# Kernel tuning notes

Hardware: AMD Instinct MI355X
Metric: run time of the kernel (lower is better)

The kernel has to match this reference:

```python
import jax, jax.numpy as jnp
import numpy as np

B, L, C, H, Wd = 256, 64, 256, 32, 32  # batch, num_filts, code_dim, height, width

def setup_inputs() -> dict:
    key = jax.random.key(0)
    k1, k2 = jax.random.split(key)
    code = jax.random.normal(k1, (B, L, C), dtype=jnp.float32)
    # stacked per-filter weights: weights[l].weight has shape [code_dim, H*W]
    W = jax.random.normal(k2, (L, C, H * Wd), dtype=jnp.float32) * (1.0 / np.sqrt(C))
    return {"code": code, "W": W}

def reference(code, W):
    # Original: for each filter l, x_hat[:, l] = code[:, l, :] @ weights[l].weight
    # (F.linear(x, weight.t()) == x @ weight). Fuse into one batched GEMM.
    # code: [B, L, C], W: [L, C, HW] -> out: [B, L, HW]
    x_hat = jnp.einsum('blc,lcd->bld', code, W)
    return x_hat.reshape(code.shape[0], W.shape[0], H, Wd)
```

## Files before the change

### kernel.cpp

```cpp
#include <hip/hip_runtime.h>
#include <hip/hip_bf16.h>

#define B_  256
#define L_  64
#define C_  256
#define HW_ 1024

typedef float  floatx4 __attribute__((ext_vector_type(4)));
typedef __bf16 bf16x8  __attribute__((ext_vector_type(8)));
typedef __bf16 bf16x4  __attribute__((ext_vector_type(4)));

#define LDT_A 72
#define LDB_ROW 128

#define BARRIER_LDS() asm volatile("s_waitcnt lgkmcnt(0)\n\ts_barrier" ::: "memory")

__device__ __forceinline__ int bswz(int n) { return (n ^ (n >> 2)) & 7; }

__global__ __launch_bounds__(512, 4)
void gld_mfma_kernel(const float* __restrict__ code,
                     const float* __restrict__ W,
                     float* __restrict__ out)
{
    const int tid = threadIdx.x;

    const int id  = blockIdx.x;
    const int ll  = id & 7;
    const int inr = id >> 3;
    const int m0  = (inr & 1) * 128;
    const int n0  = ((inr >> 1) & 7) * 128;
    const int l   = (inr >> 4) * 8 + ll;

    __shared__ __bf16 Alds[128 * LDT_A];
    __shared__ unsigned char Blds[128 * LDB_ROW];

    const int lane = tid & 63;
    const int wave = tid >> 6;
    const int wm = (wave >> 2) * 64;
    const int wn = (wave & 3) * 32;

    floatx4 acc[4][2];
    #pragma unroll
    for (int i = 0; i < 4; ++i)
        #pragma unroll
        for (int j = 0; j < 2; ++j)
            acc[i][j] = (floatx4)0.0f;

    const int a_row = tid >> 4;
    const int a_kc  = (tid & 15) * 4;
    const int b_i  = tid & 31;
    const int b_c8 = tid >> 5;

    const float* aBase = code + (size_t)m0 * (L_ * C_) + (size_t)l * C_ + a_kc;
    const float* wBase = W + (size_t)l * (C_ * HW_) + (size_t)(4 * b_c8) * HW_ + n0 + 4 * b_i;

    floatx4 Areg[4];
    floatx4 Breg[2][4];

    #pragma unroll
    for (int p = 0; p < 4; ++p)
        Areg[p] = *(const floatx4*)(aBase + (size_t)(p * 32 + a_row) * (L_ * C_));
    #pragma unroll
    for (int r = 0; r < 4; ++r)
        Breg[0][r] = *(const floatx4*)(wBase + (size_t)r * HW_);
    #pragma unroll
    for (int r = 0; r < 4; ++r)
        Breg[1][r] = *(const floatx4*)(wBase + (size_t)(64 + r) * HW_);

    int bwaddr[4];
    #pragma unroll
    for (int j = 0; j < 4; ++j) {
        const int row = 4 * b_i + j;
        bwaddr[j] = row * LDB_ROW + (((b_c8 >> 1) ^ bswz(row)) << 4) + ((b_c8 & 1) << 3);
    }

    #pragma unroll
    for (int kb = 0; kb < C_; kb += 64) {
        const int pb = (kb >> 6) & 1;

        #pragma unroll
        for (int j = 0; j < 4; ++j) {
            bf16x4 h;
            h.x = (__bf16)Breg[pb][0][j]; h.y = (__bf16)Breg[pb][1][j];
            h.z = (__bf16)Breg[pb][2][j]; h.w = (__bf16)Breg[pb][3][j];
            *(bf16x4*)&Blds[bwaddr[j]] = h;
        }
        #pragma unroll
        for (int p = 0; p < 4; ++p) {
            bf16x4 h;
            h.x = (__bf16)Areg[p].x; h.y = (__bf16)Areg[p].y;
            h.z = (__bf16)Areg[p].z; h.w = (__bf16)Areg[p].w;
            *(bf16x4*)&Alds[(p * 32 + a_row) * LDT_A + a_kc] = h;
        }

        if (kb + 64 < C_) {
            #pragma unroll
            for (int p = 0; p < 4; ++p)
                Areg[p] = *(const floatx4*)(aBase + (size_t)(p * 32 + a_row) * (L_ * C_) + (kb + 64));
        }
        if (kb + 128 < C_) {
            #pragma unroll
            for (int r = 0; r < 4; ++r)
                Breg[pb][r] = *(const floatx4*)(wBase + (size_t)(kb + 128 + r) * HW_);
        }

        BARRIER_LDS();

        #pragma unroll
        for (int ks = 0; ks < 2; ++ks) {
            bf16x8 af[4], bfr[2];
            const int koff = ks * 32 + (lane >> 4) * 8;
            #pragma unroll
            for (int i = 0; i < 4; ++i)
                af[i] = *(const bf16x8*)&Alds[(wm + i * 16 + (lane & 15)) * LDT_A + koff];
            #pragma unroll
            for (int j = 0; j < 2; ++j) {
                const int n = wn + j * 16 + (lane & 15);
                bfr[j] = *(const bf16x8*)&Blds[n * LDB_ROW + (((koff >> 3) ^ bswz(n)) << 4)];
            }
            #pragma unroll
            for (int i = 0; i < 4; ++i)
                #pragma unroll
                for (int j = 0; j < 2; ++j)
                    acc[i][j] = __builtin_amdgcn_mfma_f32_16x16x32_bf16(af[i], bfr[j], acc[i][j], 0, 0, 0);
        }

        BARRIER_LDS();
    }

    const int col0 = lane & 15;
    const int row0 = (lane >> 4) * 4;
    #pragma unroll
    for (int i = 0; i < 4; ++i) {
        #pragma unroll
        for (int j = 0; j < 2; ++j) {
            const int m = m0 + wm + i * 16 + row0;
            const int n = n0 + wn + j * 16 + col0;
            float* o = out + (size_t)m * (L_ * HW_) + (size_t)l * HW_ + n;
            #pragma unroll
            for (int r = 0; r < 4; ++r)
                o[(size_t)r * (L_ * HW_)] = acc[i][j][r];
        }
    }
}

extern "C" void kernel_launch(void* const* d_in, const int* in_sizes, int n_in,
                              void* d_out, int out_size, void* d_ws, size_t ws_size,
                              hipStream_t stream) {
    const float* code = (const float*)d_in[0];
    const float* W    = (const float*)d_in[1];
    float* out        = (float*)d_out;

    gld_mfma_kernel<<<dim3(1024), 512, 0, stream>>>(code, W, out);
}
```

Measured before the change: 133.7 us.

## Enlarge block tile to 256x256 covering full batch per filter

Each block now computes all 256 batch rows and 256 output columns for one filter, with each wave holding a 128x64 accumulator tile. This removes redundant global reads of code and W across blocks and raises MFMA work per LDS load. A is moved to the swizzled LDS layout used for B. In exchange the grid shrinks to 256 blocks with larger register and LDS use, which lowers occupancy, and W prefetch depth drops to a single stage.

Result: slower. 139.5 us (+4.4%).

```diff
diff --git a/kernel.cpp b/kernel.cpp
--- a/kernel.cpp
+++ b/kernel.cpp
@@ -10,40 +10,39 @@
 typedef __bf16 bf16x8  __attribute__((ext_vector_type(8)));
 typedef __bf16 bf16x4  __attribute__((ext_vector_type(4)));
 
-#define LDT_A 72
-#define LDB_ROW 128
-
 #define BARRIER_LDS() asm volatile("s_waitcnt lgkmcnt(0)\n\ts_barrier" ::: "memory")
 
 __device__ __forceinline__ int bswz(int n) { return (n ^ (n >> 2)) & 7; }
+__device__ __forceinline__ int lds_addr(int row, int c16, int off) {
+    return row * 128 + ((c16 ^ bswz(row)) << 4) + off;
+}
 
-__global__ __launch_bounds__(512, 4)
+__global__ __launch_bounds__(512, 2)
 void gld_mfma_kernel(const float* __restrict__ code,
                      const float* __restrict__ W,
                      float* __restrict__ out)
 {
     const int tid = threadIdx.x;
 
-    const int id  = blockIdx.x;
-    const int ll  = id & 7;
-    const int inr = id >> 3;
-    const int m0  = (inr & 1) * 128;
-    const int n0  = ((inr >> 1) & 7) * 128;
-    const int l   = (inr >> 4) * 8 + ll;
+    const int id   = blockIdx.x;
+    const int ll   = id & 7;
+    const int rest = id >> 3;
+    const int n0   = (rest & 3) * 256;
+    const int l    = (rest >> 2) * 8 + ll;
 
-    __shared__ __bf16 Alds[128 * LDT_A];
-    __shared__ unsigned char Blds[128 * LDB_ROW];
+    __shared__ unsigned char Alds[256 * 128];
+    __shared__ unsigned char Blds[256 * 128];
 
     const int lane = tid & 63;
     const int wave = tid >> 6;
-    const int wm = (wave >> 2) * 64;
-    const int wn = (wave & 3) * 32;
+    const int wm = (wave >> 2) * 128;
+    const int wn = (wave & 3) * 64;
 
-    floatx4 acc[4][2];
+    floatx4 acc[8][4];
     #pragma unroll
-    for (int i = 0; i < 4; ++i)
+    for (int i = 0; i < 8; ++i)
         #pragma unroll
-        for (int j = 0; j < 2; ++j)
+        for (int j = 0; j < 4; ++j)
             acc[i][j] = (floatx4)0.0f;
 
     const int a_row = tid >> 4;
@@ -51,77 +50,70 @@
     const int b_i  = tid & 31;
     const int b_c8 = tid >> 5;
 
-    const float* aBase = code + (size_t)m0 * (L_ * C_) + (size_t)l * C_ + a_kc;
+    const float* aBase = code + (size_t)l * C_ + a_kc;
     const float* wBase = W + (size_t)l * (C_ * HW_) + (size_t)(4 * b_c8) * HW_ + n0 + 4 * b_i;
 
-    floatx4 Areg[4];
+    floatx4 Areg[8];
     floatx4 Breg[2][4];
 
     #pragma unroll
-    for (int p = 0; p < 4; ++p)
+    for (int p = 0; p < 8; ++p)
         Areg[p] = *(const floatx4*)(aBase + (size_t)(p * 32 + a_row) * (L_ * C_));
     #pragma unroll
-    for (int r = 0; r < 4; ++r)
-        Breg[0][r] = *(const floatx4*)(wBase + (size_t)r * HW_);
-    #pragma unroll
-    for (int r = 0; r < 4; ++r)
-        Breg[1][r] = *(const floatx4*)(wBase + (size_t)(64 + r) * HW_);
-
-    int bwaddr[4];
-    #pragma unroll
-    for (int j = 0; j < 4; ++j) {
-        const int row = 4 * b_i + j;
-        bwaddr[j] = row * LDB_ROW + (((b_c8 >> 1) ^ bswz(row)) << 4) + ((b_c8 & 1) << 3);
-    }
+    for (int nh = 0; nh < 2; ++nh)
+        #pragma unroll
+        for (int r = 0; r < 4; ++r)
+            Breg[nh][r] = *(const floatx4*)(wBase + (size_t)r * HW_ + nh * 128);
 
     #pragma unroll
     for (int kb = 0; kb < C_; kb += 64) {
-        const int pb = (kb >> 6) & 1;
-
         #pragma unroll
-        for (int j = 0; j < 4; ++j) {
-            bf16x4 h;
-            h.x = (__bf16)Breg[pb][0][j]; h.y = (__bf16)Breg[pb][1][j];
-            h.z = (__bf16)Breg[pb][2][j]; h.w = (__bf16)Breg[pb][3][j];
-            *(bf16x4*)&Blds[bwaddr[j]] = h;
-        }
-        #pragma unroll
-        for (int p = 0; p < 4; ++p) {
+        for (int p = 0; p < 8; ++p) {
             bf16x4 h;
             h.x = (__bf16)Areg[p].x; h.y = (__bf16)Areg[p].y;
             h.z = (__bf16)Areg[p].z; h.w = (__bf16)Areg[p].w;
-            *(bf16x4*)&Alds[(p * 32 + a_row) * LDT_A + a_kc] = h;
+            *(bf16x4*)&Alds[lds_addr(p * 32 + a_row, a_kc >> 3, (a_kc & 4) << 1)] = h;
+        }
+        #pragma unroll
+        for (int nh = 0; nh < 2; ++nh) {
+            #pragma unroll
+            for (int j = 0; j < 4; ++j) {
+                bf16x4 h;
+                h.x = (__bf16)Breg[nh][0][j]; h.y = (__bf16)Breg[nh][1][j];
+                h.z = (__bf16)Breg[nh][2][j]; h.w = (__bf16)Breg[nh][3][j];
+                const int row = 4 * (b_i + 32 * nh) + j;
+                *(bf16x4*)&Blds[lds_addr(row, b_c8 >> 1, (b_c8 & 1) << 3)] = h;
+            }
         }
 
         if (kb + 64 < C_) {
             #pragma unroll
-            for (int p = 0; p < 4; ++p)
+            for (int p = 0; p < 8; ++p)
                 Areg[p] = *(const floatx4*)(aBase + (size_t)(p * 32 + a_row) * (L_ * C_) + (kb + 64));
-        }
-        if (kb + 128 < C_) {
             #pragma unroll
-            for (int r = 0; r < 4; ++r)
-                Breg[pb][r] = *(const floatx4*)(wBase + (size_t)(kb + 128 + r) * HW_);
+            for (int nh = 0; nh < 2; ++nh)
+                #pragma unroll
+                for (int r = 0; r < 4; ++r)
+                    Breg[nh][r] = *(const floatx4*)(wBase + (size_t)(kb + 64 + r) * HW_ + nh * 128);
         }
 
         BARRIER_LDS();
 
         #pragma unroll
         for (int ks = 0; ks < 2; ++ks) {
-            bf16x8 af[4], bfr[2];
+            bf16x8 af[8], bfr[4];
             const int koff = ks * 32 + (lane >> 4) * 8;
+            const int c16  = koff >> 3;
             #pragma unroll
-            for (int i = 0; i < 4; ++i)
-                af[i] = *(const bf16x8*)&Alds[(wm + i * 16 + (lane & 15)) * LDT_A + koff];
+            for (int i = 0; i < 8; ++i)
+                af[i] = *(const bf16x8*)&Alds[lds_addr(wm + i * 16 + (lane & 15), c16, 0)];
             #pragma unroll
-            for (int j = 0; j < 2; ++j) {
-                const int n = wn + j * 16 + (lane & 15);
-                bfr[j] = *(const bf16x8*)&Blds[n * LDB_ROW + (((koff >> 3) ^ bswz(n)) << 4)];
-            }
+            for (int j = 0; j < 4; ++j)
+                bfr[j] = *(const bf16x8*)&Blds[lds_addr(wn + j * 16 + (lane & 15), c16, 0)];
             #pragma unroll
-            for (int i = 0; i < 4; ++i)
+            for (int i = 0; i < 8; ++i)
                 #pragma unroll
-                for (int j = 0; j < 2; ++j)
+                for (int j = 0; j < 4; ++j)
                     acc[i][j] = __builtin_amdgcn_mfma_f32_16x16x32_bf16(af[i], bfr[j], acc[i][j], 0, 0, 0);
         }
 
@@ -131,10 +123,10 @@
     const int col0 = lane & 15;
     const int row0 = (lane >> 4) * 4;
     #pragma unroll
-    for (int i = 0; i < 4; ++i) {
+    for (int i = 0; i < 8; ++i) {
         #pragma unroll
-        for (int j = 0; j < 2; ++j) {
-            const int m = m0 + wm + i * 16 + row0;
+        for (int j = 0; j < 4; ++j) {
+            const int m = wm + i * 16 + row0;
             const int n = n0 + wn + j * 16 + col0;
             float* o = out + (size_t)m * (L_ * HW_) + (size_t)l * HW_ + n;
             #pragma unroll
@@ -151,5 +143,5 @@
     const float* W    = (const float*)d_in[1];
     float* out        = (float*)d_out;
 
-    gld_mfma_kernel<<<dim3(1024), 512, 0, stream>>>(code, W, out);
+    gld_mfma_kernel<<<dim3(256), 512, 0, stream>>>(code, W, out);
 }
```

## Use 128-deep K tiles with swizzled LDS for both A and B

Applied to the files above, without the earlier changes.

Doubles the K step per iteration from 64 to 128, cutting the main loop to two iterations and halving the number of barrier pairs. Both A and B tiles now use a 256-byte-row XOR-swizzled LDS layout in place of the padded A layout, and B is written as 8-wide bf16 vectors. The register prefetch changes from double-buffered B to a single 8-register A and B set loaded one full tile ahead. Register use and LDS grow to 64 KB per block, which may lower occupancy below the requested 4 blocks per CU.

New measurement: 159.8 us. 19.5% more time.

```diff
diff --git a/kernel.cpp b/kernel.cpp
--- a/kernel.cpp
+++ b/kernel.cpp
@@ -10,12 +10,12 @@
 typedef __bf16 bf16x8  __attribute__((ext_vector_type(8)));
 typedef __bf16 bf16x4  __attribute__((ext_vector_type(4)));
 
-#define LDT_A 72
-#define LDB_ROW 128
-
 #define BARRIER_LDS() asm volatile("s_waitcnt lgkmcnt(0)\n\ts_barrier" ::: "memory")
 
-__device__ __forceinline__ int bswz(int n) { return (n ^ (n >> 2)) & 7; }
+__device__ __forceinline__ int bswz(int r) { return (r ^ (r >> 2)) & 7; }
+__device__ __forceinline__ int lds_addr(int row, int cc) {
+    return row * 256 + ((cc & 8) << 4) + ((((cc ^ bswz(row)) & 7)) << 4);
+}
 
 __global__ __launch_bounds__(512, 4)
 void gld_mfma_kernel(const float* __restrict__ code,
@@ -31,8 +31,8 @@
     const int n0  = ((inr >> 1) & 7) * 128;
     const int l   = (inr >> 4) * 8 + ll;
 
-    __shared__ __bf16 Alds[128 * LDT_A];
-    __shared__ unsigned char Blds[128 * LDB_ROW];
+    __shared__ unsigned char Alds[128 * 256];
+    __shared__ unsigned char Blds[128 * 256];
 
     const int lane = tid & 63;
     const int wave = tid >> 6;
@@ -46,78 +46,64 @@
         for (int j = 0; j < 2; ++j)
             acc[i][j] = (floatx4)0.0f;
 
-    const int a_row = tid >> 4;
-    const int a_kc  = (tid & 15) * 4;
-    const int b_i  = tid & 31;
-    const int b_c8 = tid >> 5;
+    const int a_t    = tid & 31;
+    const int a_row8 = tid >> 5;
+    const int b_i = tid & 31;
+    const int b_k = tid >> 5;
 
-    const float* aBase = code + (size_t)m0 * (L_ * C_) + (size_t)l * C_ + a_kc;
-    const float* wBase = W + (size_t)l * (C_ * HW_) + (size_t)(4 * b_c8) * HW_ + n0 + 4 * b_i;
+    const float* aBase = code + (size_t)m0 * (L_ * C_) + (size_t)l * C_ + 4 * a_t;
+    const float* wBase = W + (size_t)l * (C_ * HW_) + (size_t)(8 * b_k) * HW_ + n0 + 4 * b_i;
 
-    floatx4 Areg[4];
-    floatx4 Breg[2][4];
+    floatx4 Areg[8];
+    floatx4 Breg[8];
 
     #pragma unroll
-    for (int p = 0; p < 4; ++p)
-        Areg[p] = *(const floatx4*)(aBase + (size_t)(p * 32 + a_row) * (L_ * C_));
+    for (int p = 0; p < 8; ++p)
+        Areg[p] = *(const floatx4*)(aBase + (size_t)(p * 16 + a_row8) * (L_ * C_));
     #pragma unroll
-    for (int r = 0; r < 4; ++r)
-        Breg[0][r] = *(const floatx4*)(wBase + (size_t)r * HW_);
-    #pragma unroll
-    for (int r = 0; r < 4; ++r)
-        Breg[1][r] = *(const floatx4*)(wBase + (size_t)(64 + r) * HW_);
-
-    int bwaddr[4];
-    #pragma unroll
-    for (int j = 0; j < 4; ++j) {
-        const int row = 4 * b_i + j;
-        bwaddr[j] = row * LDB_ROW + (((b_c8 >> 1) ^ bswz(row)) << 4) + ((b_c8 & 1) << 3);
-    }
+    for (int r = 0; r < 8; ++r)
+        Breg[r] = *(const floatx4*)(wBase + (size_t)r * HW_);
 
     #pragma unroll
-    for (int kb = 0; kb < C_; kb += 64) {
-        const int pb = (kb >> 6) & 1;
-
+    for (int kb = 0; kb < C_; kb += 128) {
         #pragma unroll
-        for (int j = 0; j < 4; ++j) {
-            bf16x4 h;
-            h.x = (__bf16)Breg[pb][0][j]; h.y = (__bf16)Breg[pb][1][j];
-            h.z = (__bf16)Breg[pb][2][j]; h.w = (__bf16)Breg[pb][3][j];
-            *(bf16x4*)&Blds[bwaddr[j]] = h;
-        }
-        #pragma unroll
-        for (int p = 0; p < 4; ++p) {
+        for (int p = 0; p < 8; ++p) {
             bf16x4 h;
             h.x = (__bf16)Areg[p].x; h.y = (__bf16)Areg[p].y;
             h.z = (__bf16)Areg[p].z; h.w = (__bf16)Areg[p].w;
-            *(bf16x4*)&Alds[(p * 32 + a_row) * LDT_A + a_kc] = h;
+            *(bf16x4*)&Alds[lds_addr(p * 16 + a_row8, a_t >> 1) + ((a_t & 1) << 3)] = h;
+        }
+        #pragma unroll
+        for (int j = 0; j < 4; ++j) {
+            bf16x8 h;
+            h[0] = (__bf16)Breg[0][j]; h[1] = (__bf16)Breg[1][j];
+            h[2] = (__bf16)Breg[2][j]; h[3] = (__bf16)Breg[3][j];
+            h[4] = (__bf16)Breg[4][j]; h[5] = (__bf16)Breg[5][j];
+            h[6] = (__bf16)Breg[6][j]; h[7] = (__bf16)Breg[7][j];
+            *(bf16x8*)&Blds[lds_addr(4 * b_i + j, b_k)] = h;
         }
 
-        if (kb + 64 < C_) {
-            #pragma unroll
-            for (int p = 0; p < 4; ++p)
-                Areg[p] = *(const floatx4*)(aBase + (size_t)(p * 32 + a_row) * (L_ * C_) + (kb + 64));
-        }
         if (kb + 128 < C_) {
             #pragma unroll
-            for (int r = 0; r < 4; ++r)
-                Breg[pb][r] = *(const floatx4*)(wBase + (size_t)(kb + 128 + r) * HW_);
+            for (int p = 0; p < 8; ++p)
+                Areg[p] = *(const floatx4*)(aBase + (size_t)(p * 16 + a_row8) * (L_ * C_) + (kb + 128));
+            #pragma unroll
+            for (int r = 0; r < 8; ++r)
+                Breg[r] = *(const floatx4*)(wBase + (size_t)(kb + 128 + r) * HW_);
         }
 
         BARRIER_LDS();
 
         #pragma unroll
-        for (int ks = 0; ks < 2; ++ks) {
+        for (int ks = 0; ks < 4; ++ks) {
             bf16x8 af[4], bfr[2];
-            const int koff = ks * 32 + (lane >> 4) * 8;
+            const int cc = ks * 4 + (lane >> 4);
             #pragma unroll
             for (int i = 0; i < 4; ++i)
-                af[i] = *(const bf16x8*)&Alds[(wm + i * 16 + (lane & 15)) * LDT_A + koff];
+                af[i] = *(const bf16x8*)&Alds[lds_addr(wm + i * 16 + (lane & 15), cc)];
             #pragma unroll
-            for (int j = 0; j < 2; ++j) {
-                const int n = wn + j * 16 + (lane & 15);
-                bfr[j] = *(const bf16x8*)&Blds[n * LDB_ROW + (((koff >> 3) ^ bswz(n)) << 4)];
-            }
+            for (int j = 0; j < 2; ++j)
+                bfr[j] = *(const bf16x8*)&Blds[lds_addr(wn + j * 16 + (lane & 15), cc)];
             #pragma unroll
             for (int i = 0; i < 4; ++i)
                 #pragma unroll
```
